# Performance work log

Measured on AMD Instinct MI355X. Metric: run time of the kernel, lower is better.

Reference implementation:

```python
import jax, jax.numpy as jnp
import numpy as np

B, D, H, W, C = 2, 8, 56, 56, 384
NH = 12
HD = C // NH
WIN = (2, 7, 7)
SHIFT = (1, 3, 3)
TDIM = 384
RANK = C // 8
HID = 4 * C
N = WIN[0] * WIN[1] * WIN[2]  # 98 tokens per window
NW = (D // WIN[0]) * (H // WIN[1]) * (W // WIN[2])  # windows per batch element


def _rel_index():
    wd, wh, ww = WIN
    coords = np.stack(np.meshgrid(np.arange(wd), np.arange(wh), np.arange(ww), indexing='ij'))
    coords = coords.reshape(3, -1)  # (3, N)
    rel = (coords[:, :, None] - coords[:, None, :]).transpose(1, 2, 0)  # (N, N, 3)
    rel[..., 0] += wd - 1; rel[..., 1] += wh - 1; rel[..., 2] += ww - 1
    rel[..., 0] *= (2 * wh - 1) * (2 * ww - 1)
    rel[..., 1] *= (2 * ww - 1)
    return rel.sum(-1)  # (N, N) int

REL_IDX = _rel_index()


def _wpart_np(x):
    b, d, h, w, c = x.shape
    x = x.reshape(b, d // WIN[0], WIN[0], h // WIN[1], WIN[1], w // WIN[2], WIN[2], c)
    return x.transpose(0, 1, 3, 5, 2, 4, 6, 7).reshape(-1, N, c)


def _attn_mask():
    # faithful port of compute_mask (note: only 2 slices along W, as in source)
    wd, wh, ww = WIN
    sd, sh, sw = SHIFT
    img = np.zeros((1, D, H, W, 1), np.float32)
    cnt = 0
    for ds in (slice(-wd), slice(-wd, -sd), slice(-sd, None)):
        for hs in (slice(-wh), slice(-wh, -sh), slice(-sh, None)):
            for ws in (slice(-ww), slice(-ww, None)):
                img[:, ds, hs, ws, :] = cnt
                cnt += 1
    mw = _wpart_np(img).squeeze(-1)  # (nW, N)
    am = mw[:, None, :] - mw[:, :, None]  # (nW, N, N)
    return np.where(am != 0, np.float32(-100.0), np.float32(0.0))

ATTN_MASK = _attn_mask()


def wpart(x):
    b, c = x.shape[0], x.shape[-1]
    x = x.reshape(b, D // WIN[0], WIN[0], H // WIN[1], WIN[1], W // WIN[2], WIN[2], c)
    return x.transpose(0, 1, 3, 5, 2, 4, 6, 7).reshape(-1, N, c)


def wrev(win):
    c = win.shape[-1]
    x = win.reshape(B, D // WIN[0], H // WIN[1], W // WIN[2], WIN[0], WIN[1], WIN[2], c)
    return x.transpose(0, 1, 4, 2, 5, 3, 6, 7).reshape(B, D, H, W, c)


def ln(x):
    m = x.mean(-1, keepdims=True)
    v = ((x - m) ** 2).mean(-1, keepdims=True)
    return (x - m) / jnp.sqrt(v + 1e-6)


def window_attn(xw, qkv_w, qkv_b, proj_w, proj_b, rel_bias, mask):
    Bw = xw.shape[0]
    qkv = (xw @ qkv_w + qkv_b).reshape(Bw, N, 3, NH, HD).transpose(2, 0, 3, 1, 4)
    q, k, v = qkv[0] * (HD ** -0.5), qkv[1], qkv[2]
    a = jnp.einsum('bhnd,bhmd->bhnm', q, k)  # (Bw, NH, N, N)
    bias = rel_bias[REL_IDX.reshape(-1)].reshape(N, N, NH).transpose(2, 0, 1)
    a = a + bias[None]
    a = a.reshape(Bw // NW, NW, NH, N, N) + mask[None, :, None]
    a = jax.nn.softmax(a.reshape(Bw, NH, N, N), axis=-1)
    out = jnp.einsum('bhnm,bhmd->bhnd', a, v).transpose(0, 2, 1, 3).reshape(Bw, N, C)
    return out @ proj_w + proj_b


def setup_inputs() -> dict:
    key = jax.random.key(0)
    ks = jax.random.split(key, 16)
    s = 0.02
    return {
        'x': jax.random.normal(ks[0], (B, D, H, W, C), jnp.float32),
        't': jax.random.normal(ks[1], (B, TDIM), jnp.float32),
        'qkv_w': jax.random.normal(ks[2], (C, 3 * C), jnp.float32) * s,
        'qkv_b': jax.random.normal(ks[3], (3 * C,), jnp.float32) * s,
        'proj_w': jax.random.normal(ks[4], (C, C), jnp.float32) * s,
        'proj_b': jax.random.normal(ks[5], (C,), jnp.float32) * s,
        'rel_bias': jax.random.normal(ks[6], ((2 * WIN[0] - 1) * (2 * WIN[1] - 1) * (2 * WIN[2] - 1), NH), jnp.float32) * s,
        'fc1_w': jax.random.normal(ks[7], (C, HID), jnp.float32) * s,
        'fc1_b': jax.random.normal(ks[8], (HID,), jnp.float32) * s,
        'fc2_w': jax.random.normal(ks[9], (HID, C), jnp.float32) * s,
        'fc2_b': jax.random.normal(ks[10], (C,), jnp.float32) * s,
        'ada_w1': jax.random.normal(ks[11], (TDIM, RANK), jnp.float32) * s,
        'ada_w2': jax.random.normal(ks[12], (RANK, 6 * C), jnp.float32) * s,
        'ada_b2': jax.random.normal(ks[13], (6 * C,), jnp.float32) * s,
    }


def reference(x, t, qkv_w, qkv_b, proj_w, proj_b, rel_bias, fc1_w, fc1_b, fc2_w, fc2_b, ada_w1, ada_w2, ada_b2):
    mask = jnp.asarray(ATTN_MASK)
    mod = jax.nn.silu(t) @ ada_w1 @ ada_w2 + ada_b2  # (B, 6C)
    s_msa, sc_msa, g_msa, s_mlp, sc_mlp, g_mlp = jnp.split(mod, 6, axis=1)

    def mod5(h, sh, sc):
        return h * (1 + sc[:, None, None, None, :]) + sh[:, None, None, None, :]

    # attention branch (shifted-window MSA)
    h = mod5(ln(x), s_msa, sc_msa)
    hs = jnp.roll(h, shift=(-SHIFT[0], -SHIFT[1], -SHIFT[2]), axis=(1, 2, 3))
    aw = window_attn(wpart(hs), qkv_w, qkv_b, proj_w, proj_b, rel_bias, mask)
    hs = wrev(aw)
    h = jnp.roll(hs, shift=SHIFT, axis=(1, 2, 3))
    x = x + g_msa[:, None, None, None, :] * h

    # MLP branch
    h2 = mod5(ln(x), s_mlp, sc_mlp)
    m = jax.nn.gelu(h2 @ fc1_w + fc1_b, approximate=False) @ fc2_w + fc2_b
    return x + g_mlp[:, None, None, None, :] * m
```

## Files before the change

### kernel.cpp

```cpp
#include <hip/hip_runtime.h>
#include <hip/hip_bf16.h>
#include <math.h>

using bf16 = __hip_bfloat16;
typedef __bf16 bf16x8 __attribute__((ext_vector_type(8)));
typedef float f32x4 __attribute__((ext_vector_type(4)));
typedef unsigned int u32;


__device__ __forceinline__ void async_cp16(const void* g, void* l) {
  __builtin_amdgcn_global_load_lds(
      (const __attribute__((address_space(1))) u32*)g,
      (__attribute__((address_space(3))) u32*)l, 16, 0, 0);
}

__device__ __forceinline__ int row_to_gidx(int row) {
  int win = row / 98, tok = row - win * 98;
  int b = win >> 8, wd = (win >> 6) & 3, wh = (win >> 3) & 7, ww = win & 7;
  int td = tok / 49, rem = tok - td * 49;
  int th = rem / 7, tw = rem - th * 7;
  int od = (wd * 2 + td + 1) & 7;
  int oh = wh * 7 + th + 3; if (oh >= 56) oh -= 56;
  int ow = ww * 7 + tw + 3; if (ow >= 56) ow -= 56;
  return ((b * 8 + od) * 56 + oh) * 56 + ow;
}

__global__ __launch_bounds__(256) void mod_kernel(
    const float* __restrict__ t, const float* __restrict__ w1,
    const float* __restrict__ w2, const float* __restrict__ b2,
    float* __restrict__ modout)
{
  __shared__ float u[2 * 48];
  int tid = threadIdx.x;
  if (tid < 96) {
    int b = tid / 48, r = tid - (tid / 48) * 48;
    float acc = 0.f;
    for (int k = 0; k < 384; ++k) {
      float x = t[b * 384 + k];
      float s = x / (1.f + __expf(-x));
      acc += s * w1[k * 48 + r];
    }
    u[b * 48 + r] = acc;
  }
  __syncthreads();
  for (int idx = tid; idx < 2 * 2304; idx += 256) {
    int b = idx / 2304, c = idx - b * 2304;
    float acc = b2[c];
    #pragma unroll
    for (int k = 0; k < 48; ++k) acc += u[b * 48 + k] * w2[k * 2304 + c];
    modout[idx] = acc;
  }
}

__global__ __launch_bounds__(256) void wconv_frag_kernel(
    const float* __restrict__ W, bf16* __restrict__ Wf, int K, int N)
{
  int idx = blockIdx.x * 256 + threadIdx.x;
  if (idx >= K * N) return;
  int k = idx / N, n = idx - (idx / N) * N;
  int ntile = n >> 4, kstep = k >> 5;
  int l = (n & 15) + (((k >> 3) & 3) << 4);
  size_t dst = (((size_t)(ntile * (K >> 5) + kstep)) << 9) + (l << 3) + (k & 7);
  Wf[dst] = __float2bfloat16(W[idx]);
}

__global__ __launch_bounds__(256) void bm_kernel(
    const float* __restrict__ relb, bf16* __restrict__ bm)
{
  int idx = blockIdx.x * 256 + threadIdx.x;
  if (idx >= 4 * 12 * 112 * 112) return;
  int j = idx % 112, tmp = idx / 112;
  int i = tmp % 112; tmp /= 112;
  int h = tmp % 12, p = tmp / 12;
  float v;
  if (i < 98 && j < 98) {
    int tdi = i / 49, ri = i % 49, thi = ri / 7, twi = ri % 7;
    int tdj = j / 49, rj = j % 49, thj = rj / 7, twj = rj % 7;
    int ridx = (tdi - tdj + 1) * 169 + (thi - thj + 6) * 13 + (twi - twj + 6);
    bool msk = ((p & 2) && (tdi != tdj)) || ((p & 1) && ((thi < 4) != (thj < 4)));
    v = relb[ridx * 12 + h] + (msk ? -100.f : 0.f);
  } else {
    v = -1e38f;
  }
  bm[idx] = __float2bfloat16(v);
}

template <int PHASE>
__global__ __launch_bounds__(256) void ln_mod_kernel(
    const float* __restrict__ src, const float* __restrict__ modv,
    bf16* __restrict__ dst)
{
  int wid = threadIdx.x >> 6, lane = threadIdx.x & 63;
  int row = blockIdx.x * 4 + wid;
  int gtok;
  if (PHASE == 0) gtok = row_to_gidx(row); else gtok = row;
  int b = row / 25088;
  const float* s = src + (size_t)gtok * 384;
  float vals[6], sum = 0.f, sq = 0.f;
  #pragma unroll
  for (int i = 0; i < 6; ++i) {
    float v = s[lane + i * 64];
    vals[i] = v; sum += v; sq += v * v;
  }
  #pragma unroll
  for (int o = 32; o; o >>= 1) { sum += __shfl_xor(sum, o, 64); sq += __shfl_xor(sq, o, 64); }
  float mean = sum * (1.f / 384.f);
  float var = sq * (1.f / 384.f) - mean * mean;
  float rstd = rsqrtf(var + 1e-6f);
  int mb = b * 2304 + (PHASE == 0 ? 0 : 1152);
  #pragma unroll
  for (int i = 0; i < 6; ++i) {
    int c = lane + i * 64;
    float scv = modv[mb + 384 + c], shv = modv[mb + c];
    dst[(size_t)row * 384 + c] = __float2bfloat16((vals[i] - mean) * rstd * (1.f + scv) + shv);
  }
}

template <int EPI>
__global__ __launch_bounds__(256) void gemm128_kernel(
    const bf16* __restrict__ A, const bf16* __restrict__ Bf,
    const float* __restrict__ bias, const int N, const int K,
    bf16* __restrict__ outB, float* __restrict__ outF,
    const float* __restrict__ resid, const float* __restrict__ modv)
{
  __shared__ bf16 sA[4][128 * 32];
  const int tid = threadIdx.x;
  const int lane = tid & 63, wid = tid >> 6;
  const int wm = wid >> 1, wn = wid & 1;

  const int gx = gridDim.x;
  const int nwg = gx * (int)gridDim.y;
  const int orig = (int)blockIdx.y * gx + (int)blockIdx.x;
  const int q = nwg >> 3;
  const int wg = (orig & 7) * q + (orig >> 3);
  const int bx = wg % gx, by = wg / gx;
  const int row0 = by * 128, col0 = bx * 128;

  const int lrow = lane & 15;
  const int sl8 = (((lane >> 4) ^ ((lane >> 1) & 3)) << 3);
  const int r0 = tid >> 2;
  const int c0 = (((tid & 3) ^ ((tid >> 3) & 3)) << 3);

  const int nK32 = K >> 5;
  const bf16* Bfb[4];
  #pragma unroll
  for (int n = 0; n < 4; ++n) {
    const int ntile = (col0 >> 4) + wn * 4 + n;
    Bfb[n] = Bf + (((size_t)(ntile * nK32)) << 9) + (lane << 3);
  }

  const f32x4 vzero = {0.f, 0.f, 0.f, 0.f};
  f32x4 acc[4][4];
  #pragma unroll
  for (int m = 0; m < 4; ++m)
    #pragma unroll
    for (int n = 0; n < 4; ++n) acc[m][n] = vzero;

  const bf16* Arow0 = A + (size_t)(row0 + r0) * K + c0;
  const bf16* Arow1 = A + (size_t)(row0 + r0 + 64) * K + c0;

  auto stage = [&](int b, int kt) {
    async_cp16(Arow0 + kt, &sA[b][(size_t)tid * 8]);
    async_cp16(Arow1 + kt, &sA[b][(size_t)(tid + 256) * 8]);
  };

  stage(0, 0);
  stage(1, 32);
  for (int t = 0; t < nK32; ++t) {
    if (t + 2 < nK32) stage((t + 2) & 3, (t + 2) * 32);
    const int younger = nK32 - 1 - t;
    if (younger >= 2)      asm volatile("s_waitcnt vmcnt(4)" ::: "memory");
    else if (younger == 1) asm volatile("s_waitcnt vmcnt(2)" ::: "memory");
    else                   asm volatile("s_waitcnt vmcnt(0)" ::: "memory");
    __builtin_amdgcn_s_barrier();

    bf16x8 bfv[4], af[4];
    #pragma unroll
    for (int n = 0; n < 4; ++n)
      bfv[n] = *(const bf16x8*)(Bfb[n] + ((size_t)t << 9));
    #pragma unroll
    for (int m = 0; m < 4; ++m)
      af[m] = *(const bf16x8*)(&sA[t & 3][(wm * 64 + m * 16 + lrow) * 32 + sl8]);
    #pragma unroll
    for (int m = 0; m < 4; ++m)
      #pragma unroll
      for (int n = 0; n < 4; ++n)
        acc[m][n] = __builtin_amdgcn_mfma_f32_16x16x32_bf16(af[m], bfv[n], acc[m][n], 0, 0, 0);
  }

  #pragma unroll
  for (int m = 0; m < 4; ++m) {
    #pragma unroll
    for (int r = 0; r < 4; ++r) {
      const int row = row0 + wm * 64 + m * 16 + (lane >> 4) * 4 + r;
      int gofs = 0, b = 0;
      if (EPI == 1) { gofs = row_to_gidx(row) * 384; b = row / 25088; }
      if (EPI == 3) { gofs = row * 384; b = row / 25088; }
      #pragma unroll
      for (int n = 0; n < 4; ++n) {
        const int col = col0 + wn * 64 + n * 16 + (lane & 15);
        float v = acc[m][n][r] + bias[col];
        if (EPI == 0) {
          outB[(size_t)row * N + col] = __float2bfloat16(v);
        } else if (EPI == 2) {
          float g = 0.5f * v * (1.f + erff(v * 0.70710678118654752f));
          outB[(size_t)row * N + col] = __float2bfloat16(g);
        } else if (EPI == 1) {
          outF[gofs + col] = resid[gofs + col] + modv[b * 2304 + 768 + col] * v;
        } else {
          outF[gofs + col] = resid[gofs + col] + modv[b * 2304 + 1920 + col] * v;
        }
      }
    }
  }
}

__global__ __launch_bounds__(256) void attn_kernel(
    const bf16* __restrict__ qkv, const bf16* __restrict__ bm,
    bf16* __restrict__ outp)
{
  __shared__ bf16 k_s[112][40];
  __shared__ bf16 v_t[32][136];
  __shared__ bf16 p_s[4][16][136];

  const int head = blockIdx.x;
  const int win = blockIdx.y;
  const int tid = threadIdx.x;
  const int lane = tid & 63, wid = tid >> 6;
  const int g = lane >> 4, c16 = lane & 15;
  const size_t rowbase = (size_t)win * 98;
  const bf16 zero = __float2bfloat16(0.f);

  for (int lin = tid; lin < 448; lin += 256) {
    int row = lin >> 2, ch = (lin & 3) << 3;
    uint4 val = make_uint4(0, 0, 0, 0);
    if (row < 98)
      val = *(const uint4*)(qkv + (rowbase + row) * 1152 + 384 + head * 32 + ch);
    *(uint4*)&k_s[row][ch] = val;
  }
  for (int lin = tid; lin < 4096; lin += 256) {
    int d = lin & 31, tok = lin >> 5;
    bf16 val = zero;
    if (tok < 98) val = qkv[(rowbase + tok) * 1152 + 768 + head * 32 + d];
    v_t[d][tok] = val;
  }
  for (int lin = tid; lin < 1536; lin += 256) {
    int w = lin / 384, rem = lin - w * 384;
    p_s[w][rem / 24][112 + rem % 24] = zero;
  }
  __syncthreads();

  const int p = ((((win >> 6) & 3) == 3) ? 2 : 0) | ((((win >> 3) & 7) == 7) ? 1 : 0);
  const bf16* bmrow = bm + (size_t)(p * 12 + head) * 12544;
  const float scale = 0.17677669529663687f;
  const f32x4 vzero = {0.f, 0.f, 0.f, 0.f};

  for (int s = wid; s < 7; s += 4) {
    const int q0 = s * 16;
    int qrow = q0 + c16; if (qrow > 97) qrow = 97;
    bf16x8 qf = *(const bf16x8*)(qkv + (rowbase + qrow) * 1152 + head * 32 + g * 8);

    f32x4 sa[7];
    #pragma unroll
    for (int ct = 0; ct < 7; ++ct) {
      bf16x8 kf = *(const bf16x8*)&k_s[ct * 16 + c16][g * 8];
      sa[ct] = __builtin_amdgcn_mfma_f32_16x16x32_bf16(qf, kf, vzero, 0, 0, 0);
    }

    float sv[7][4];
    float mrow[4] = {-1e30f, -1e30f, -1e30f, -1e30f};
    #pragma unroll
    for (int ct = 0; ct < 7; ++ct) {
      #pragma unroll
      for (int r = 0; r < 4; ++r) {
        int i = q0 + g * 4 + r, j = ct * 16 + c16;
        float val = sa[ct][r] * scale + __bfloat162float(bmrow[i * 112 + j]);
        sv[ct][r] = val;
        mrow[r] = fmaxf(mrow[r], val);
      }
    }
    #pragma unroll
    for (int r = 0; r < 4; ++r) {
      #pragma unroll
      for (int off = 1; off < 16; off <<= 1)
        mrow[r] = fmaxf(mrow[r], __shfl_xor(mrow[r], off, 64));
    }
    float rsum[4] = {0.f, 0.f, 0.f, 0.f};
    #pragma unroll
    for (int ct = 0; ct < 7; ++ct) {
      #pragma unroll
      for (int r = 0; r < 4; ++r) {
        float e = __expf(sv[ct][r] - mrow[r]);
        sv[ct][r] = e;
        rsum[r] += e;
      }
    }
    #pragma unroll
    for (int r = 0; r < 4; ++r) {
      #pragma unroll
      for (int off = 1; off < 16; off <<= 1)
        rsum[r] += __shfl_xor(rsum[r], off, 64);
      rsum[r] = 1.f / rsum[r];
    }
    #pragma unroll
    for (int ct = 0; ct < 7; ++ct)
      #pragma unroll
      for (int r = 0; r < 4; ++r)
        p_s[wid][g * 4 + r][ct * 16 + c16] = __float2bfloat16(sv[ct][r] * rsum[r]);

    asm volatile("s_waitcnt lgkmcnt(0)" ::: "memory");

    f32x4 o0 = vzero, o1 = vzero;
    #pragma unroll
    for (int kk = 0; kk < 4; ++kk) {
      bf16x8 pa = *(const bf16x8*)&p_s[wid][c16][kk * 32 + g * 8];
      bf16x8 v0 = *(const bf16x8*)&v_t[c16][kk * 32 + g * 8];
      bf16x8 v1 = *(const bf16x8*)&v_t[16 + c16][kk * 32 + g * 8];
      o0 = __builtin_amdgcn_mfma_f32_16x16x32_bf16(pa, v0, o0, 0, 0, 0);
      o1 = __builtin_amdgcn_mfma_f32_16x16x32_bf16(pa, v1, o1, 0, 0, 0);
    }
    #pragma unroll
    for (int r = 0; r < 4; ++r) {
      int qi = q0 + g * 4 + r;
      if (qi < 98) {
        size_t ob = (rowbase + qi) * 384 + head * 32;
        outp[ob + c16] = __float2bfloat16(o0[r]);
        outp[ob + 16 + c16] = __float2bfloat16(o1[r]);
      }
    }
  }
}

extern "C" void kernel_launch(void* const* d_in, const int* in_sizes, int n_in,
                              void* d_out, int out_size, void* d_ws, size_t ws_size,
                              hipStream_t stream)
{
  (void)in_sizes; (void)n_in; (void)out_size; (void)ws_size;
  const float* x      = (const float*)d_in[0];
  const float* t      = (const float*)d_in[1];
  const float* qkv_w  = (const float*)d_in[2];
  const float* qkv_b  = (const float*)d_in[3];
  const float* proj_w = (const float*)d_in[4];
  const float* proj_b = (const float*)d_in[5];
  const float* relb   = (const float*)d_in[6];
  const float* fc1_w  = (const float*)d_in[7];
  const float* fc1_b  = (const float*)d_in[8];
  const float* fc2_w  = (const float*)d_in[9];
  const float* fc2_b  = (const float*)d_in[10];
  const float* ada_w1 = (const float*)d_in[11];
  const float* ada_w2 = (const float*)d_in[12];
  const float* ada_b2 = (const float*)d_in[13];
  float* out = (float*)d_out;
  char* ws = (char*)d_ws;

  float* modbuf = (float*)(ws + 0);
  bf16* wqkv_t  = (bf16*)(ws + 18432);
  bf16* wproj_t = (bf16*)(ws + 903168);
  bf16* wfc1_t  = (bf16*)(ws + 1198080);
  bf16* wfc2_t  = (bf16*)(ws + 2377728);
  bf16* bufA    = (bf16*)(ws + 3557376);
  bf16* qkvbuf  = (bf16*)(ws + 42092544);
  bf16* bufB    = (bf16*)(ws + 42092544 + 115605504);
  bf16* midbuf  = (bf16*)(ws + 42092544);
  bf16* bmbuf   = bufA;

  wconv_frag_kernel<<<(384 * 1152 + 255) / 256, 256, 0, stream>>>(qkv_w, wqkv_t, 384, 1152);
  wconv_frag_kernel<<<(384 * 384 + 255) / 256, 256, 0, stream>>>(proj_w, wproj_t, 384, 384);
  wconv_frag_kernel<<<(384 * 1536 + 255) / 256, 256, 0, stream>>>(fc1_w, wfc1_t, 384, 1536);
  wconv_frag_kernel<<<(1536 * 384 + 255) / 256, 256, 0, stream>>>(fc2_w, wfc2_t, 1536, 384);

  mod_kernel<<<1, 256, 0, stream>>>(t, ada_w1, ada_w2, ada_b2, modbuf);

  ln_mod_kernel<0><<<12544, 256, 0, stream>>>(x, modbuf, bufA);

  gemm128_kernel<0><<<dim3(9, 392), 256, 0, stream>>>(bufA, wqkv_t, qkv_b, 1152, 384,
                                                      qkvbuf, nullptr, nullptr, nullptr);

  bm_kernel<<<2352, 256, 0, stream>>>(relb, bmbuf);

  attn_kernel<<<dim3(12, 512), 256, 0, stream>>>(qkvbuf, bmbuf, bufB);

  gemm128_kernel<1><<<dim3(3, 392), 256, 0, stream>>>(bufB, wproj_t, proj_b, 384, 384,
                                                      nullptr, out, x, modbuf);

  ln_mod_kernel<1><<<12544, 256, 0, stream>>>(out, modbuf, bufA);

  gemm128_kernel<2><<<dim3(12, 392), 256, 0, stream>>>(bufA, wfc1_t, fc1_b, 1536, 384,
                                                       midbuf, nullptr, nullptr, nullptr);

  gemm128_kernel<3><<<dim3(3, 392), 256, 0, stream>>>(midbuf, wfc2_t, fc2_b, 384, 1536,
                                                      nullptr, out, out, modbuf);
}
```

Before: 560.7 us.

## Fuse MLP fc1, GELU and fc2 into one kernel keeping hidden in LDS

Replaces the two MLP GEMM launches with one fused kernel. Each workgroup holds a 64-row input tile in LDS, computes 128-column chunks of fc1 with GELU into a double-buffered LDS tile, and accumulates fc2 directly in registers. This removes the write and re-read of the 50176x1536 bf16 hidden activation in global memory. In exchange each workgroup streams the full weight matrices from global memory or cache, and the large accumulator register footprint may limit occupancy.

```diff
diff --git a/kernel.cpp b/kernel.cpp
--- a/kernel.cpp
+++ b/kernel.cpp
@@ -195,21 +195,129 @@
       const int row = row0 + wm * 64 + m * 16 + (lane >> 4) * 4 + r;
       int gofs = 0, b = 0;
       if (EPI == 1) { gofs = row_to_gidx(row) * 384; b = row / 25088; }
-      if (EPI == 3) { gofs = row * 384; b = row / 25088; }
       #pragma unroll
       for (int n = 0; n < 4; ++n) {
         const int col = col0 + wn * 64 + n * 16 + (lane & 15);
         float v = acc[m][n][r] + bias[col];
         if (EPI == 0) {
           outB[(size_t)row * N + col] = __float2bfloat16(v);
-        } else if (EPI == 2) {
-          float g = 0.5f * v * (1.f + erff(v * 0.70710678118654752f));
-          outB[(size_t)row * N + col] = __float2bfloat16(g);
-        } else if (EPI == 1) {
+        } else {
           outF[gofs + col] = resid[gofs + col] + modv[b * 2304 + 768 + col] * v;
-        } else {
-          outF[gofs + col] = resid[gofs + col] + modv[b * 2304 + 1920 + col] * v;
         }
+      }
+    }
+  }
+}
+
+__global__ __launch_bounds__(256, 2) void mlp_kernel(
+    const bf16* __restrict__ A, const bf16* __restrict__ W1f,
+    const float* __restrict__ b1, const bf16* __restrict__ W2f,
+    const float* __restrict__ b2, const float* __restrict__ resid,
+    const float* __restrict__ modv, float* __restrict__ outF)
+{
+  __shared__ bf16 sA[64 * 384];
+  __shared__ bf16 sP[2][64 * 128];
+
+  const int tid = threadIdx.x;
+  const int lane = tid & 63, wid = tid >> 6;
+  const int c16 = lane & 15, g = lane >> 4;
+
+  const int nwg = gridDim.x;
+  const int orig = blockIdx.x;
+  const int q = nwg >> 3;
+  const int wg = (orig & 7) * q + (orig >> 3);
+  const int row0 = wg * 64;
+  const int bb = row0 / 25088;
+
+  #pragma unroll
+  for (int i = 0; i < 12; ++i) {
+    int L = tid + i * 256;
+    int row = L / 48, p = L - (L / 48) * 48;
+    int s = p ^ (row & 7);
+    async_cp16(A + (size_t)(row0 + row) * 384 + s * 8, sA + (size_t)L * 8);
+  }
+  asm volatile("s_waitcnt vmcnt(0)" ::: "memory");
+  __syncthreads();
+
+  const f32x4 vzero = {0.f, 0.f, 0.f, 0.f};
+  f32x4 acc2[4][6];
+  #pragma unroll
+  for (int m = 0; m < 4; ++m)
+    #pragma unroll
+    for (int j = 0; j < 6; ++j) acc2[m][j] = vzero;
+
+  for (int ch = 0; ch < 12; ++ch) {
+    f32x4 acc1[4][2];
+    #pragma unroll
+    for (int m = 0; m < 4; ++m) { acc1[m][0] = vzero; acc1[m][1] = vzero; }
+    const bf16* w1p0 = W1f + (((size_t)((ch * 8 + wid * 2 + 0) * 12)) << 9) + (lane << 3);
+    const bf16* w1p1 = W1f + (((size_t)((ch * 8 + wid * 2 + 1) * 12)) << 9) + (lane << 3);
+    #pragma unroll
+    for (int ks = 0; ks < 12; ++ks) {
+      bf16x8 bf0 = *(const bf16x8*)(w1p0 + ((size_t)ks << 9));
+      bf16x8 bf1 = *(const bf16x8*)(w1p1 + ((size_t)ks << 9));
+      bf16x8 af[4];
+      #pragma unroll
+      for (int m = 0; m < 4; ++m) {
+        int row = m * 16 + c16;
+        int phys = (ks * 4 + g) ^ (row & 7);
+        af[m] = *(const bf16x8*)(sA + row * 384 + phys * 8);
+      }
+      #pragma unroll
+      for (int m = 0; m < 4; ++m) {
+        acc1[m][0] = __builtin_amdgcn_mfma_f32_16x16x32_bf16(af[m], bf0, acc1[m][0], 0, 0, 0);
+        acc1[m][1] = __builtin_amdgcn_mfma_f32_16x16x32_bf16(af[m], bf1, acc1[m][1], 0, 0, 0);
+      }
+    }
+    bf16* sp = sP[ch & 1];
+    #pragma unroll
+    for (int j = 0; j < 2; ++j) {
+      const int colc = (wid * 2 + j) * 16 + c16;
+      const float bias1 = b1[ch * 128 + colc];
+      #pragma unroll
+      for (int m = 0; m < 4; ++m) {
+        #pragma unroll
+        for (int r = 0; r < 4; ++r) {
+          const int row = m * 16 + g * 4 + r;
+          float v = acc1[m][j][r] + bias1;
+          float gl = 0.5f * v * (1.f + erff(v * 0.70710678118654752f));
+          const int half = row * 128 + (((((colc >> 3) ^ (row & 7))) << 3) | (colc & 7));
+          sp[half] = __float2bfloat16(gl);
+        }
+      }
+    }
+    __syncthreads();
+    #pragma unroll
+    for (int ks = 0; ks < 4; ++ks) {
+      bf16x8 af2[4];
+      #pragma unroll
+      for (int m = 0; m < 4; ++m) {
+        int row = m * 16 + c16;
+        int phys = (ks * 4 + g) ^ (row & 7);
+        af2[m] = *(const bf16x8*)(sp + row * 128 + phys * 8);
+      }
+      #pragma unroll
+      for (int j = 0; j < 6; ++j) {
+        const bf16* w2p = W2f + (((size_t)((wid * 6 + j) * 48 + ch * 4 + ks)) << 9) + (lane << 3);
+        bf16x8 bf2 = *(const bf16x8*)w2p;
+        #pragma unroll
+        for (int m = 0; m < 4; ++m)
+          acc2[m][j] = __builtin_amdgcn_mfma_f32_16x16x32_bf16(af2[m], bf2, acc2[m][j], 0, 0, 0);
+      }
+    }
+  }
+
+  #pragma unroll
+  for (int m = 0; m < 4; ++m) {
+    #pragma unroll
+    for (int r = 0; r < 4; ++r) {
+      const int row = row0 + m * 16 + g * 4 + r;
+      const size_t gofs = (size_t)row * 384;
+      #pragma unroll
+      for (int j = 0; j < 6; ++j) {
+        const int col = (wid * 6 + j) * 16 + c16;
+        float v = acc2[m][j][r] + b2[col];
+        outF[gofs + col] = resid[gofs + col] + modv[bb * 2304 + 1920 + col] * v;
       }
     }
   }
@@ -361,7 +469,6 @@
   bf16* bufA    = (bf16*)(ws + 3557376);
   bf16* qkvbuf  = (bf16*)(ws + 42092544);
   bf16* bufB    = (bf16*)(ws + 42092544 + 115605504);
-  bf16* midbuf  = (bf16*)(ws + 42092544);
   bf16* bmbuf   = bufA;
 
   wconv_frag_kernel<<<(384 * 1152 + 255) / 256, 256, 0, stream>>>(qkv_w, wqkv_t, 384, 1152);
@@ -385,9 +492,6 @@
 
   ln_mod_kernel<1><<<12544, 256, 0, stream>>>(out, modbuf, bufA);
 
-  gemm128_kernel<2><<<dim3(12, 392), 256, 0, stream>>>(bufA, wfc1_t, fc1_b, 1536, 384,
-                                                       midbuf, nullptr, nullptr, nullptr);
-
-  gemm128_kernel<3><<<dim3(3, 392), 256, 0, stream>>>(midbuf, wfc2_t, fc2_b, 384, 1536,
-                                                      nullptr, out, out, modbuf);
-}
+  mlp_kernel<<<784, 256, 0, stream>>>(bufA, wfc1_t, fc1_b, wfc2_t, fc2_b,
+                                      out, modbuf, out);
+}
```

After: 621.4 us. 1.11x slower.

## Prefetch B fragments one step ahead, transpose MFMA operands for vectorized epilogue

Applied to the files above, without the earlier changes.

The GEMM main loop is unrolled by two, and the next K step's B fragments are loaded into a second register set while the current step computes, which hides global-load latency for B. The MFMA operand order is swapped so each lane holds four consecutive columns of one row. The epilogue can then use 4-wide vector loads and stores for bias, residual, modulation and output. The XCD workgroup remap also now handles workgroup counts not divisible by 8. The cost is more registers and waitcnt bookkeeping that has to be exact.

```diff
diff --git a/kernel.cpp b/kernel.cpp
--- a/kernel.cpp
+++ b/kernel.cpp
@@ -4,6 +4,7 @@
 
 using bf16 = __hip_bfloat16;
 typedef __bf16 bf16x8 __attribute__((ext_vector_type(8)));
+typedef __bf16 bf16x4 __attribute__((ext_vector_type(4)));
 typedef float f32x4 __attribute__((ext_vector_type(4)));
 typedef unsigned int u32;
 
@@ -131,8 +132,9 @@
   const int gx = gridDim.x;
   const int nwg = gx * (int)gridDim.y;
   const int orig = (int)blockIdx.y * gx + (int)blockIdx.x;
-  const int q = nwg >> 3;
-  const int wg = (orig & 7) * q + (orig >> 3);
+  const int q = nwg >> 3, rr = nwg & 7;
+  const int xcd = orig & 7, idx = orig >> 3;
+  const int wg = (xcd < rr ? xcd * (q + 1) : rr * (q + 1) + (xcd - rr) * q) + idx;
   const int bx = wg % gx, by = wg / gx;
   const int row0 = by * 128, col0 = bx * 128;
 
@@ -164,52 +166,92 @@
     async_cp16(Arow1 + kt, &sA[b][(size_t)(tid + 256) * 8]);
   };
 
+  bf16x8 b0[4], b1[4];
+
+#define LOADB(dst, t)                                                         \
+  {                                                                           \
+    _Pragma("unroll")                                                         \
+    for (int n = 0; n < 4; ++n)                                               \
+      dst[n] = *(const bf16x8*)(Bfb[n] + ((size_t)(t) << 9));                 \
+  }
+#define COMPUTE(cb, bb)                                                       \
+  {                                                                           \
+    bf16x8 af[4];                                                             \
+    _Pragma("unroll")                                                         \
+    for (int m = 0; m < 4; ++m)                                               \
+      af[m] = *(const bf16x8*)(&sA[cb][(wm * 64 + m * 16 + lrow) * 32 + sl8]);\
+    _Pragma("unroll")                                                         \
+    for (int m = 0; m < 4; ++m)                                               \
+      _Pragma("unroll")                                                       \
+      for (int n = 0; n < 4; ++n)                                             \
+        acc[m][n] = __builtin_amdgcn_mfma_f32_16x16x32_bf16(bb[n], af[m],     \
+                                                            acc[m][n], 0, 0, 0); \
+  }
+
+  LOADB(b0, 0);
   stage(0, 0);
   stage(1, 32);
-  for (int t = 0; t < nK32; ++t) {
-    if (t + 2 < nK32) stage((t + 2) & 3, (t + 2) * 32);
-    const int younger = nK32 - 1 - t;
-    if (younger >= 2)      asm volatile("s_waitcnt vmcnt(4)" ::: "memory");
-    else if (younger == 1) asm volatile("s_waitcnt vmcnt(2)" ::: "memory");
-    else                   asm volatile("s_waitcnt vmcnt(0)" ::: "memory");
+
+  for (int t = 0; t < nK32; t += 2) {
+    if (t + 1 < nK32) LOADB(b1, t + 1);
+    if (t + 2 < nK32) {
+      stage((t + 2) & 3, (t + 2) * 32);
+      asm volatile("s_waitcnt vmcnt(8)" ::: "memory");
+    } else {
+      asm volatile("s_waitcnt vmcnt(6)" ::: "memory");
+    }
     __builtin_amdgcn_s_barrier();
-
-    bf16x8 bfv[4], af[4];
-    #pragma unroll
-    for (int n = 0; n < 4; ++n)
-      bfv[n] = *(const bf16x8*)(Bfb[n] + ((size_t)t << 9));
-    #pragma unroll
-    for (int m = 0; m < 4; ++m)
-      af[m] = *(const bf16x8*)(&sA[t & 3][(wm * 64 + m * 16 + lrow) * 32 + sl8]);
-    #pragma unroll
-    for (int m = 0; m < 4; ++m)
-      #pragma unroll
-      for (int n = 0; n < 4; ++n)
-        acc[m][n] = __builtin_amdgcn_mfma_f32_16x16x32_bf16(af[m], bfv[n], acc[m][n], 0, 0, 0);
-  }
-
+    COMPUTE(t & 3, b0);
+    if (t + 2 < nK32) LOADB(b0, t + 2);
+    if (t + 3 < nK32) {
+      stage((t + 3) & 3, (t + 3) * 32);
+      asm volatile("s_waitcnt vmcnt(8)" ::: "memory");
+    } else if (t + 2 < nK32) {
+      asm volatile("s_waitcnt vmcnt(6)" ::: "memory");
+    } else {
+      asm volatile("s_waitcnt vmcnt(0)" ::: "memory");
+    }
+    __builtin_amdgcn_s_barrier();
+    COMPUTE((t + 1) & 3, b1);
+  }
+#undef LOADB
+#undef COMPUTE
+
+  const int cg = (lane >> 4) << 2;
   #pragma unroll
   for (int m = 0; m < 4; ++m) {
-    #pragma unroll
-    for (int r = 0; r < 4; ++r) {
-      const int row = row0 + wm * 64 + m * 16 + (lane >> 4) * 4 + r;
-      int gofs = 0, b = 0;
-      if (EPI == 1) { gofs = row_to_gidx(row) * 384; b = row / 25088; }
-      if (EPI == 3) { gofs = row * 384; b = row / 25088; }
-      #pragma unroll
-      for (int n = 0; n < 4; ++n) {
-        const int col = col0 + wn * 64 + n * 16 + (lane & 15);
-        float v = acc[m][n][r] + bias[col];
-        if (EPI == 0) {
-          outB[(size_t)row * N + col] = __float2bfloat16(v);
-        } else if (EPI == 2) {
-          float g = 0.5f * v * (1.f + erff(v * 0.70710678118654752f));
-          outB[(size_t)row * N + col] = __float2bfloat16(g);
-        } else if (EPI == 1) {
-          outF[gofs + col] = resid[gofs + col] + modv[b * 2304 + 768 + col] * v;
-        } else {
-          outF[gofs + col] = resid[gofs + col] + modv[b * 2304 + 1920 + col] * v;
+    const int row = row0 + wm * 64 + m * 16 + lrow;
+    int gofs = 0, b = 0;
+    if (EPI == 1) { gofs = row_to_gidx(row) * 384; b = row / 25088; }
+    if (EPI == 3) { gofs = row * 384; b = row / 25088; }
+    #pragma unroll
+    for (int n = 0; n < 4; ++n) {
+      const int colb = col0 + wn * 64 + n * 16 + cg;
+      const f32x4 bi = *(const f32x4*)(bias + colb);
+      f32x4 v;
+      #pragma unroll
+      for (int r = 0; r < 4; ++r) v[r] = acc[m][n][r] + bi[r];
+      if (EPI == 0) {
+        bf16x4 pk;
+        #pragma unroll
+        for (int r = 0; r < 4; ++r) pk[r] = (__bf16)v[r];
+        *(bf16x4*)(outB + (size_t)row * N + colb) = pk;
+      } else if (EPI == 2) {
+        bf16x4 pk;
+        #pragma unroll
+        for (int r = 0; r < 4; ++r) {
+          float g = 0.5f * v[r] * (1.f + erff(v[r] * 0.70710678118654752f));
+          pk[r] = (__bf16)g;
         }
+        *(bf16x4*)(outB + (size_t)row * N + colb) = pk;
+      } else {
+        const int mo = b * 2304 + (EPI == 1 ? 768 : 1920);
+        const f32x4 res = *(const f32x4*)(resid + gofs + colb);
+        const f32x4 gm = *(const f32x4*)(modv + mo + colb);
+        f32x4 o;
+        #pragma unroll
+        for (int r = 0; r < 4; ++r) o[r] = res[r] + gm[r] * v[r];
+        *(f32x4*)(outF + gofs + colb) = o;
       }
     }
   }
```

Measured after the change: 616.6 us. 10.0% more time.
